# Performance work log

Hardware: AMD Instinct MI355X
Metric: run time of the kernel (lower is better)

Reference implementation:

```python
import jax, jax.numpy as jnp
import numpy as np

E = 1024
H = 16
D = E // H
B = 4
NQ = 4096
NK = 4096
LN_EPS = 1e-5


def setup_inputs() -> dict:
    key = jax.random.key(0)
    ks = jax.random.split(key, 16)
    s = 1.0 / np.sqrt(E)
    return {
        "query_embed": jax.random.normal(ks[0], (B, NQ, E), jnp.float32),
        "key_embed": jax.random.normal(ks[1], (B, NK, E), jnp.float32),
        "value": jax.random.normal(ks[2], (B, NK, E), jnp.float32),
        "Wq": jax.random.normal(ks[3], (E, E), jnp.float32) * s,
        "bq": jax.random.normal(ks[4], (E,), jnp.float32) * s,
        "Wk": jax.random.normal(ks[5], (E, E), jnp.float32) * s,
        "bk": jax.random.normal(ks[6], (E,), jnp.float32) * s,
        "Wv": jax.random.normal(ks[7], (E, E), jnp.float32) * s,
        "bv": jax.random.normal(ks[8], (E,), jnp.float32) * s,
        "Wo": jax.random.normal(ks[9], (E, E), jnp.float32) * s,
        "bo": jax.random.normal(ks[10], (E,), jnp.float32) * s,
        "gq": jnp.ones((E,), jnp.float32),
        "betaq": jnp.zeros((E,), jnp.float32),
        "gk": jnp.ones((E,), jnp.float32),
        "betak": jnp.zeros((E,), jnp.float32),
    }


def _layernorm(x, g, b):
    mu = jnp.mean(x, axis=-1, keepdims=True)
    var = jnp.mean(jnp.square(x - mu), axis=-1, keepdims=True)
    return (x - mu) * jax.lax.rsqrt(var + LN_EPS) * g + b


def reference(query_embed, key_embed, value, Wq, bq, Wk, bk, Wv, bv, Wo, bo,
              gq, betaq, gk, betak):
    Bq, Nq, _ = query_embed.shape
    _, Nk, _ = key_embed.shape
    # projections (torch Linear: x @ W.T + b) + LayerNorm
    q = _layernorm(query_embed @ Wq.T + bq, gq, betaq).reshape(Bq, Nq, H, D)
    k = _layernorm(key_embed @ Wk.T + bk, gk, betak).reshape(Bq, Nk, H, D)
    v = (value @ Wv.T + bv).reshape(Bq, Nk, H, D)
    # elu + 1 feature map
    q = jax.nn.elu(q) + 1.0  # [B, Nq, H, D]
    k = jax.nn.elu(k) + 1.0  # [B, Nk, H, D]
    # linear attention: O(N*d^2)
    kv_sum = jnp.einsum('bnhd,bnhe->bhde', k, v)        # [B, H, D, D]
    k_sum = jnp.sum(k, axis=1)                          # [B, H, D]
    num = jnp.einsum('bqhd,bhde->bqhe', q, kv_sum)      # [B, Nq, H, D]
    den = jnp.einsum('bqhd,bhd->bqh', q, k_sum)[..., None] + 1e-8
    out = (num / den).reshape(Bq, Nq, H * D)
    return out @ Wo.T + bo
```

## Files before the change

kernel.cpp:

```cpp
#include <hip/hip_runtime.h>
#include <hip/hip_bf16.h>

#define EDIM 1024
#define HHEADS 16
#define DHEAD 64
#define BB 4
#define NSEQ 4096
#define NTOK 16384
#define KVSPLIT 16

typedef unsigned short u16;
using frag8 = __attribute__((ext_vector_type(8))) short;
using facc4 = __attribute__((ext_vector_type(4))) float;

__device__ __forceinline__ float b2f(u16 u) {
  union { unsigned int i; float f; } c; c.i = ((unsigned int)u) << 16; return c.f;
}
__device__ __forceinline__ u16 f2b(float f) {
  __hip_bfloat16 h = __float2bfloat16(f);
  union { __hip_bfloat16 h; u16 u; } c; c.h = h; return c.u;
}
__device__ __forceinline__ void gl2lds16(const void* g, void* l) {
  __builtin_amdgcn_global_load_lds(
      (const __attribute__((address_space(1))) unsigned int*)g,
      (__attribute__((address_space(3))) unsigned int*)l, 16, 0, 0);
}

__global__ void detect_dtype(const u16* __restrict__ src, unsigned* __restrict__ flag) {
  const int lane = threadIdx.x;
  const unsigned u = src[(size_t)lane * 200000];
  const unsigned e = (u >> 7) & 0xFF;
  const bool inl = (u == 0) || (e >= 100 && e <= 135);
  const unsigned long long m = __ballot(inl);
  if (lane == 0) flag[0] = (__popcll(m) >= 32) ? 1u : 0u;
}

__global__ __launch_bounds__(256) void cvt_bf16(
    const void* __restrict__ src, u16* __restrict__ dst, int n,
    const unsigned* __restrict__ flag) {
  if (flag[0] == 1) return;
  const int i0 = (blockIdx.x * 256 + threadIdx.x) * 8;
  if (i0 >= n) return;
  const float4 a = ((const float4*)src)[i0 >> 2];
  const float4 b = ((const float4*)src)[(i0 >> 2) + 1];
  ushort4 lo, hi;
  lo.x = f2b(a.x); lo.y = f2b(a.y); lo.z = f2b(a.z); lo.w = f2b(a.w);
  hi.x = f2b(b.x); hi.y = f2b(b.y); hi.z = f2b(b.z); hi.w = f2b(b.w);
  ((ushort4*)dst)[i0 >> 2] = lo;
  ((ushort4*)dst)[(i0 >> 2) + 1] = hi;
}

struct Ptr8 { const void* s[8]; u16* d[8]; };
__global__ __launch_bounds__(256) void cvt8(Ptr8 p, const unsigned* __restrict__ flag) {
  const int t = blockIdx.x * 256 + threadIdx.x;
  const int v = t >> 7;
  const int i0 = (t & 127) * 8;
  const void* s = p.s[v];
  u16* d = p.d[v];
  ushort4 lo, hi;
  if (flag[0] == 0) {
    const float4 a = ((const float4*)s)[i0 >> 2];
    const float4 b = ((const float4*)s)[(i0 >> 2) + 1];
    lo.x = f2b(a.x); lo.y = f2b(a.y); lo.z = f2b(a.z); lo.w = f2b(a.w);
    hi.x = f2b(b.x); hi.y = f2b(b.y); hi.z = f2b(b.z); hi.w = f2b(b.w);
  } else {
    lo = ((const ushort4*)s)[i0 >> 2];
    hi = ((const ushort4*)s)[(i0 >> 2) + 1];
  }
  ((ushort4*)d)[i0 >> 2] = lo;
  ((ushort4*)d)[(i0 >> 2) + 1] = hi;
}

__global__ __launch_bounds__(256, 2) void gemm_bias(
    const void* __restrict__ Araw, const u16* __restrict__ Acvt,
    const void* __restrict__ Wraw, const u16* __restrict__ Wcvt,
    const u16* __restrict__ bias, u16* __restrict__ C,
    const unsigned* __restrict__ flag, int outMode)
{
  __shared__ __align__(16) u16 As[128 * 32];
  __shared__ __align__(16) u16 Bs[128 * 32];
  const int tid  = threadIdx.x;
  const int lane = tid & 63;
  const int w    = tid >> 6;
  const int wm   = w >> 1, wn = w & 1;
  const int rowBase = blockIdx.x * 128;
  const int colBase = blockIdx.y * 128;

  const bool bfw = (flag[0] == 1);
  const u16* A = bfw ? (const u16*)Araw : Acvt;
  const u16* W = bfw ? (const u16*)Wraw : Wcvt;

  facc4 acc[4][4];
#pragma unroll
  for (int i = 0; i < 4; ++i)
#pragma unroll
    for (int j = 0; j < 4; ++j) acc[i][j] = (facc4){0.f, 0.f, 0.f, 0.f};

  const int sRow = w * 32 + (lane >> 2);
  const int sCol = (lane & 3) * 8;
  const u16* Ag = A + (size_t)(rowBase + sRow) * EDIM + sCol;
  const u16* Wg = W + (size_t)(colBase + sRow) * EDIM + sCol;
  u16* AsB = As + w * 1024;
  u16* BsB = Bs + w * 1024;

  const int fr = lane & 15;
  const int kq = (lane >> 4) * 8;

  for (int k0 = 0; k0 < EDIM; k0 += 32) {
    gl2lds16(Ag + k0,            AsB);
    gl2lds16(Ag + k0 + 16*EDIM,  AsB + 512);
    gl2lds16(Wg + k0,            BsB);
    gl2lds16(Wg + k0 + 16*EDIM,  BsB + 512);
    __syncthreads();
    frag8 af[4], bf[4];
#pragma unroll
    for (int i = 0; i < 4; ++i)
      af[i] = *(const frag8*)(As + (wm * 64 + i * 16 + fr) * 32 + kq);
#pragma unroll
    for (int j = 0; j < 4; ++j)
      bf[j] = *(const frag8*)(Bs + (wn * 64 + j * 16 + fr) * 32 + kq);
#pragma unroll
    for (int i = 0; i < 4; ++i)
#pragma unroll
      for (int j = 0; j < 4; ++j)
        acc[i][j] = __builtin_amdgcn_mfma_f32_16x16x32_bf16(af[i], bf[j], acc[i][j], 0, 0, 0);
    __syncthreads();
  }

  const bool f32out = (outMode == 1) && !bfw;
  float* Cf = (float*)C;
  float bvv[4];
#pragma unroll
  for (int j = 0; j < 4; ++j)
    bvv[j] = b2f(bias[colBase + wn * 64 + j * 16 + fr]);
#pragma unroll
  for (int i = 0; i < 4; ++i) {
#pragma unroll
    for (int r = 0; r < 4; ++r) {
      const int row = rowBase + wm * 64 + i * 16 + (lane >> 4) * 4 + r;
      const size_t ro = (size_t)row * EDIM + colBase + wn * 64 + fr;
#pragma unroll
      for (int j = 0; j < 4; ++j) {
        const float val = acc[i][j][r] + bvv[j];
        if (f32out) Cf[ro + j * 16] = val;
        else        C[ro + j * 16]  = f2b(val);
      }
    }
  }
}

__global__ __launch_bounds__(256) void ln_elu(
    const u16* __restrict__ X, const u16* __restrict__ g,
    const u16* __restrict__ beta, u16* __restrict__ Y)
{
  __shared__ float wsum[4], wsq[4];
  const int row = blockIdx.x, tid = threadIdx.x;
  const ushort4 xu = ((const ushort4*)(X + (size_t)row * EDIM))[tid];
  float x[4] = { b2f(xu.x), b2f(xu.y), b2f(xu.z), b2f(xu.w) };
  float s  = x[0] + x[1] + x[2] + x[3];
  float ss = x[0]*x[0] + x[1]*x[1] + x[2]*x[2] + x[3]*x[3];
#pragma unroll
  for (int off = 32; off > 0; off >>= 1) {
    s  += __shfl_down(s,  off, 64);
    ss += __shfl_down(ss, off, 64);
  }
  if ((tid & 63) == 0) { wsum[tid >> 6] = s; wsq[tid >> 6] = ss; }
  __syncthreads();
  const float S  = wsum[0] + wsum[1] + wsum[2] + wsum[3];
  const float SS = wsq[0] + wsq[1] + wsq[2] + wsq[3];
  const float mu  = S * (1.0f / EDIM);
  const float var = SS * (1.0f / EDIM) - mu * mu;
  const float rs  = rsqrtf(var + 1e-5f);
  const ushort4 gu = ((const ushort4*)g)[tid];
  const ushort4 bu = ((const ushort4*)beta)[tid];
  float gg[4] = { b2f(gu.x), b2f(gu.y), b2f(gu.z), b2f(gu.w) };
  float bb[4] = { b2f(bu.x), b2f(bu.y), b2f(bu.z), b2f(bu.w) };
  ushort4 out;
  u16 o[4];
#pragma unroll
  for (int c = 0; c < 4; ++c) {
    float y = (x[c] - mu) * rs * gg[c] + bb[c];
    y = (y > 0.f) ? (y + 1.f) : __expf(y);
    o[c] = f2b(y);
  }
  out.x = o[0]; out.y = o[1]; out.z = o[2]; out.w = o[3];
  ((ushort4*)(Y + (size_t)row * EDIM))[tid] = out;
}

__global__ __launch_bounds__(256) void kv_partial(
    const u16* __restrict__ Km, const u16* __restrict__ V,
    float* __restrict__ partials, float* __restrict__ kspart)
{
  __shared__ __align__(16) u16 smem[2 * 64 * 130];
  u16 (*kT)[130] = (u16(*)[130])smem;
  u16 (*vT)[130] = (u16(*)[130])(smem + 64 * 130);
  float* red = (float*)smem;
  float* ksr = ((float*)smem) + 4352;

  const int split = blockIdx.x, h = blockIdx.y, b = blockIdx.z;
  const int bh = b * HHEADS + h;
  const int tid = threadIdx.x, lane = tid & 63, w = tid >> 6;
  const size_t base = (size_t)b * NSEQ * EDIM + h * DHEAD;
  const int nbase = split * (NSEQ / KVSPLIT);

  float ksacc[8] = {0, 0, 0, 0, 0, 0, 0, 0};
  facc4 acc[4][4];
#pragma unroll
  for (int i = 0; i < 4; ++i)
#pragma unroll
    for (int j = 0; j < 4; ++j) acc[i][j] = (facc4){0.f, 0.f, 0.f, 0.f};

  const int e0 = (tid & 7) * 8;
  const int nl0 = tid >> 3;
  const int fr = lane & 15;
  const int quad = lane >> 4;

  for (int c = 0; c < 2; ++c) {
    const int nchunk = nbase + c * 128;
#pragma unroll
    for (int rep = 0; rep < 4; ++rep) {
      const int n = rep * 32 + nl0;
      const uint4 kd = *(const uint4*)(Km + base + (size_t)(nchunk + n) * EDIM + e0);
      const uint4 vd = *(const uint4*)(V  + base + (size_t)(nchunk + n) * EDIM + e0);
      const u16* pk = (const u16*)&kd;
      const u16* pv = (const u16*)&vd;
#pragma unroll
      for (int ii = 0; ii < 8; ++ii) {
        kT[e0 + ii][n] = pk[ii];
        ksacc[ii] += b2f(pk[ii]);
        vT[e0 + ii][n] = pv[ii];
      }
    }
    __syncthreads();
    const int kq2 = w * 32 + quad * 8;
    frag8 af[4], bf[4];
#pragma unroll
    for (int i = 0; i < 4; ++i) af[i] = *(const frag8*)&kT[i * 16 + fr][kq2];
#pragma unroll
    for (int j = 0; j < 4; ++j) bf[j] = *(const frag8*)&vT[j * 16 + fr][kq2];
#pragma unroll
    for (int i = 0; i < 4; ++i)
#pragma unroll
      for (int j = 0; j < 4; ++j)
        acc[i][j] = __builtin_amdgcn_mfma_f32_16x16x32_bf16(af[i], bf[j], acc[i][j], 0, 0, 0);
    __syncthreads();
  }

  for (int p = 0; p < 4; ++p) {
    const int j = (w + p) & 3;
#pragma unroll
    for (int i = 0; i < 4; ++i)
#pragma unroll
      for (int r = 0; r < 4; ++r) {
        const int d = i * 16 + quad * 4 + r;
        const int e = j * 16 + fr;
        if (p == 0) red[d * 68 + e] = acc[i][j][r];
        else        red[d * 68 + e] += acc[i][j][r];
      }
    __syncthreads();
  }

  const size_t pbase = ((size_t)bh * KVSPLIT + split) * 4096;
#pragma unroll
  for (int ii = 0; ii < 16; ++ii) {
    const int idx = tid + ii * 256;
    partials[pbase + idx] = red[(idx >> 6) * 68 + (idx & 63)];
  }

#pragma unroll
  for (int ii = 0; ii < 8; ++ii) {
    ksacc[ii] += __shfl_down(ksacc[ii], 32, 64);
    ksacc[ii] += __shfl_down(ksacc[ii], 16, 64);
    ksacc[ii] += __shfl_down(ksacc[ii], 8, 64);
  }
  if (lane < 8) {
#pragma unroll
    for (int ii = 0; ii < 8; ++ii) ksr[w * 64 + lane * 8 + ii] = ksacc[ii];
  }
  __syncthreads();
  if (tid < 64)
    kspart[((size_t)bh * KVSPLIT + split) * 64 + tid] =
        ksr[tid] + ksr[64 + tid] + ksr[128 + tid] + ksr[192 + tid];
}

__global__ __launch_bounds__(256) void kv_reduce(
    const float* __restrict__ partials, const float* __restrict__ kspart,
    float* __restrict__ KV, float* __restrict__ Ks)
{
  const int qt = blockIdx.x;
  const int bh = blockIdx.y;
  const int tid = threadIdx.x;
#pragma unroll
  for (int ii = 0; ii < 4; ++ii) {
    const int idx = qt * 1024 + ii * 256 + tid;
    float s = 0.f;
#pragma unroll
    for (int sp = 0; sp < KVSPLIT; ++sp)
      s += partials[((size_t)bh * KVSPLIT + sp) * 4096 + idx];
    KV[(size_t)bh * 4096 + idx] = s;
  }
  if (qt == 0 && tid < 64) {
    float s = 0.f;
#pragma unroll
    for (int sp = 0; sp < KVSPLIT; ++sp)
      s += kspart[((size_t)bh * KVSPLIT + sp) * 64 + tid];
    Ks[bh * 64 + tid] = s;
  }
}

__global__ __launch_bounds__(256) void attn_nd(
    const u16* __restrict__ Q, const float* __restrict__ KV,
    const float* __restrict__ Ks, u16* __restrict__ O)
{
  __shared__ __align__(16) u16 kvT[64][72];
  __shared__ float ks_s[64];
  __shared__ float den_s[4][16];
  const int qt = blockIdx.x, h = blockIdx.y, b = blockIdx.z;
  const int bh = b * HHEADS + h;
  const int tid = threadIdx.x, lane = tid & 63, w = tid >> 6;
  const float* kvp = KV + (size_t)bh * 4096;
#pragma unroll
  for (int ii = 0; ii < 16; ++ii) {
    const int idx = tid + ii * 256;
    kvT[idx & 63][idx >> 6] = f2b(kvp[idx]);
  }
  if (tid < 64) ks_s[tid] = Ks[bh * 64 + tid];
  __syncthreads();

  const int fr = lane & 15;
  const int q8 = (lane >> 4) * 8;
  const u16* qp = Q + (size_t)(b * NSEQ + qt * 64 + w * 16 + fr) * EDIM + h * DHEAD;
  const frag8 a0 = *(const frag8*)(qp + q8);
  const frag8 a1 = *(const frag8*)(qp + 32 + q8);

  const u16* a0u = (const u16*)&a0;
  const u16* a1u = (const u16*)&a1;
  float den = 0.f;
#pragma unroll
  for (int j = 0; j < 8; ++j)
    den += b2f(a0u[j]) * ks_s[q8 + j] + b2f(a1u[j]) * ks_s[32 + q8 + j];
  den += __shfl_xor(den, 16, 64);
  den += __shfl_xor(den, 32, 64);
  if (lane < 16) den_s[w][lane] = den + 1e-8f;

  facc4 acc[4];
#pragma unroll
  for (int j = 0; j < 4; ++j) acc[j] = (facc4){0.f, 0.f, 0.f, 0.f};
#pragma unroll
  for (int j = 0; j < 4; ++j) {
    const frag8 b0 = *(const frag8*)&kvT[j * 16 + fr][q8];
    const frag8 b1 = *(const frag8*)&kvT[j * 16 + fr][32 + q8];
    acc[j] = __builtin_amdgcn_mfma_f32_16x16x32_bf16(a0, b0, acc[j], 0, 0, 0);
    acc[j] = __builtin_amdgcn_mfma_f32_16x16x32_bf16(a1, b1, acc[j], 0, 0, 0);
  }
  __syncthreads();
#pragma unroll
  for (int r = 0; r < 4; ++r) {
    const int rq = (lane >> 4) * 4 + r;
    const float dv = den_s[w][rq];
    const size_t orow = (size_t)(b * NSEQ + qt * 64 + w * 16 + rq) * EDIM + h * DHEAD;
#pragma unroll
    for (int j = 0; j < 4; ++j)
      O[orow + j * 16 + fr] = f2b(acc[j][r] / dv);
  }
}

extern "C" void kernel_launch(void* const* d_in, const int* in_sizes, int n_in,
                              void* d_out, int out_size, void* d_ws, size_t ws_size,
                              hipStream_t stream) {
  char* ws = (char*)d_ws;
  const size_t EH = (size_t)NTOK * EDIM;
  unsigned* flag = (unsigned*)ws;
  u16* Wqb  = (u16*)(ws + 1024);
  u16* Wkb  = Wqb + EDIM * EDIM;
  u16* Wvb  = Wkb + EDIM * EDIM;
  u16* Wob  = Wvb + EDIM * EDIM;
  u16* bqb  = Wob + EDIM * EDIM;
  u16* bkb  = bqb + 1024;
  u16* bvb  = bkb + 1024;
  u16* bob  = bvb + 1024;
  u16* gqb  = bob + 1024;
  u16* bEqb = gqb + 1024;
  u16* gkb  = bEqb + 1024;
  u16* bEkb = gkb + 1024;
  u16* Xin  = bEkb + 1024;
  u16* preQ = Xin + EH;
  u16* preK = preQ + EH;
  u16* vbuf = preK + EH;
  float* partials = (float*)(vbuf + EH);
  float* kspart   = partials + (size_t)64 * KVSPLIT * 4096;
  float* kvbuf    = kspart + (size_t)64 * KVSPLIT * 64;
  float* ksbuf    = kvbuf + (size_t)64 * 4096;

  const dim3 gg(NTOK / 128, EDIM / 128), tb(256);
  const int NW = EDIM * EDIM;

  detect_dtype<<<1, 64, 0, stream>>>((const u16*)d_in[0], flag);
  cvt_bf16<<<NW / 2048, 256, 0, stream>>>(d_in[3], Wqb, NW, flag);
  cvt_bf16<<<NW / 2048, 256, 0, stream>>>(d_in[5], Wkb, NW, flag);
  cvt_bf16<<<NW / 2048, 256, 0, stream>>>(d_in[7], Wvb, NW, flag);
  cvt_bf16<<<NW / 2048, 256, 0, stream>>>(d_in[9], Wob, NW, flag);
  Ptr8 p8;
  p8.s[0] = d_in[4];  p8.s[1] = d_in[6];  p8.s[2] = d_in[8];  p8.s[3] = d_in[10];
  p8.s[4] = d_in[11]; p8.s[5] = d_in[12]; p8.s[6] = d_in[13]; p8.s[7] = d_in[14];
  p8.d[0] = bqb; p8.d[1] = bkb; p8.d[2] = bvb; p8.d[3] = bob;
  p8.d[4] = gqb; p8.d[5] = bEqb; p8.d[6] = gkb; p8.d[7] = bEkb;
  cvt8<<<4, 256, 0, stream>>>(p8, flag);

  cvt_bf16<<<EH / 2048, 256, 0, stream>>>(d_in[0], Xin, (int)EH, flag);
  gemm_bias<<<gg, tb, 0, stream>>>(d_in[0], Xin, d_in[3], Wqb, bqb, preQ, flag, 0);
  cvt_bf16<<<EH / 2048, 256, 0, stream>>>(d_in[1], Xin, (int)EH, flag);
  gemm_bias<<<gg, tb, 0, stream>>>(d_in[1], Xin, d_in[5], Wkb, bkb, preK, flag, 0);
  cvt_bf16<<<EH / 2048, 256, 0, stream>>>(d_in[2], Xin, (int)EH, flag);
  gemm_bias<<<gg, tb, 0, stream>>>(d_in[2], Xin, d_in[7], Wvb, bvb, vbuf, flag, 0);

  ln_elu<<<NTOK, 256, 0, stream>>>(preQ, gqb, bEqb, preQ);
  ln_elu<<<NTOK, 256, 0, stream>>>(preK, gkb, bEkb, preK);

  kv_partial<<<dim3(KVSPLIT, HHEADS, BB), tb, 0, stream>>>(preK, vbuf, partials, kspart);
  kv_reduce<<<dim3(4, 64), tb, 0, stream>>>(partials, kspart, kvbuf, ksbuf);
  attn_nd<<<dim3(NSEQ / 64, HHEADS, BB), tb, 0, stream>>>(preQ, kvbuf, ksbuf, Xin);
  gemm_bias<<<gg, tb, 0, stream>>>(Xin, Xin, d_in[9], Wob, bob, (u16*)d_out, flag, 1);
}
```

Baseline: 554.2 us.

## Replace 128x128 GEMM with 256x256 tiled, double-buffered, swizzled 512-thread GEMM

Swaps the projection and output GEMM kernel for a 256x256 tile version with 8 waves, 64-wide K steps and double-buffered LDS quadrants. Global-to-LDS loads are issued across phases with explicit vmcnt waits, and XOR swizzling reduces LDS bank conflicts. A block index remap groups tiles for L2 locality. The aim is higher MFMA utilisation and more operand reuse across the four large GEMMs, at the cost of more LDS and registers per block and fragile hand scheduling.

```diff
diff --git a/kernel.cpp b/kernel.cpp
--- a/kernel.cpp
+++ b/kernel.cpp
@@ -71,61 +71,120 @@
   ((ushort4*)d)[(i0 >> 2) + 1] = hi;
 }
 
-__global__ __launch_bounds__(256, 2) void gemm_bias(
+#define STA(BUF, QM, T)                                                       \
+  gl2lds16(Ag + (size_t)(QM) * 64 * EDIM + (size_t)(T) * 64,                  \
+           AsW + (BUF) * 16384 + (QM) * 8192);                                \
+  gl2lds16(Ag + (size_t)(QM) * 64 * EDIM + 128 * EDIM + (size_t)(T) * 64,     \
+           AsW + (BUF) * 16384 + (QM) * 8192 + 4096);
+
+#define STB(BUF, QN, T)                                                       \
+  gl2lds16(Bg + (size_t)(QN) * 32 * EDIM + (size_t)(T) * 64,                  \
+           BsW + (BUF) * 16384 + (QN) * 8192);                                \
+  gl2lds16(Bg + (size_t)(QN) * 32 * EDIM + 128 * EDIM + (size_t)(T) * 64,     \
+           BsW + (BUF) * 16384 + (QN) * 8192 + 4096);
+
+#define VM(N) asm volatile("s_waitcnt vmcnt(" #N ")" ::: "memory");
+
+#define PH(BUF, QM, QN, ISSUE, TAIL)                                          \
+  {                                                                           \
+    frag8 af[4][2], bq[2][2];                                                 \
+    _Pragma("unroll") for (int i = 0; i < 4; ++i) {                           \
+      const u16* rp = &As[BUF][QM][wm * 64 + i * 16 + fr][0];                 \
+      af[i][0] = *(const frag8*)(rp + c0);                                    \
+      af[i][1] = *(const frag8*)(rp + c1);                                    \
+    }                                                                         \
+    _Pragma("unroll") for (int j = 0; j < 2; ++j) {                           \
+      const u16* rp = &Bs[BUF][QN][wn * 32 + j * 16 + fr][0];                 \
+      bq[j][0] = *(const frag8*)(rp + c0);                                    \
+      bq[j][1] = *(const frag8*)(rp + c1);                                    \
+    }                                                                         \
+    ISSUE                                                                     \
+    __builtin_amdgcn_s_barrier();                                             \
+    asm volatile("s_waitcnt lgkmcnt(0)" ::: "memory");                        \
+    __builtin_amdgcn_sched_barrier(0);                                        \
+    __builtin_amdgcn_s_setprio(1);                                            \
+    _Pragma("unroll") for (int kk = 0; kk < 2; ++kk)                          \
+      _Pragma("unroll") for (int i = 0; i < 4; ++i)                           \
+        _Pragma("unroll") for (int j = 0; j < 2; ++j)                         \
+          acc[(QM) * 4 + i][(QN) * 2 + j] =                                   \
+              __builtin_amdgcn_mfma_f32_16x16x32_bf16(                        \
+                  af[i][kk], bq[j][kk], acc[(QM) * 4 + i][(QN) * 2 + j],      \
+                  0, 0, 0);                                                   \
+    __builtin_amdgcn_s_setprio(0);                                            \
+    TAIL                                                                      \
+    __builtin_amdgcn_s_barrier();                                             \
+    __builtin_amdgcn_sched_barrier(0);                                        \
+  }
+
+__global__ __launch_bounds__(512, 2) void gemm256(
     const void* __restrict__ Araw, const u16* __restrict__ Acvt,
     const void* __restrict__ Wraw, const u16* __restrict__ Wcvt,
     const u16* __restrict__ bias, u16* __restrict__ C,
     const unsigned* __restrict__ flag, int outMode)
 {
-  __shared__ __align__(16) u16 As[128 * 32];
-  __shared__ __align__(16) u16 Bs[128 * 32];
+  __shared__ __align__(16) u16 As[2][2][128][64];
+  __shared__ __align__(16) u16 Bs[2][2][128][64];
+
   const int tid  = threadIdx.x;
   const int lane = tid & 63;
   const int w    = tid >> 6;
-  const int wm   = w >> 1, wn = w & 1;
-  const int rowBase = blockIdx.x * 128;
-  const int colBase = blockIdx.y * 128;
+  const int wm   = w >> 2;
+  const int wn   = w & 3;
+
+  const int bid0 = blockIdx.x;
+  const int bid  = (bid0 & 7) * 32 + (bid0 >> 3);
+  const int rowBase = (bid >> 2) * 256;
+  const int colBase = (bid & 3) * 256;
 
   const bool bfw = (flag[0] == 1);
-  const u16* A = bfw ? (const u16*)Araw : Acvt;
-  const u16* W = bfw ? (const u16*)Wraw : Wcvt;
-
-  facc4 acc[4][4];
-#pragma unroll
-  for (int i = 0; i < 4; ++i)
+  const u16* A  = bfw ? (const u16*)Araw : Acvt;
+  const u16* Wt = bfw ? (const u16*)Wraw : Wcvt;
+
+  const int lr = w * 8 + (lane >> 3);
+  const int sc = 8 * ((lane & 7) ^ (lane >> 3));
+  const u16* Ag = A  + (size_t)(rowBase + lr) * EDIM + sc;
+  const u16* Bg = Wt + (size_t)(colBase + (lr >> 5) * 64 + (lr & 31)) * EDIM + sc;
+  u16* AsW = &As[0][0][w * 8][0];
+  u16* BsW = &Bs[0][0][w * 8][0];
+
+  const int fr = lane & 15;
+  const int qd = lane >> 4;
+  const int sw = fr & 7;
+  const int c0 = 8 * (qd ^ sw);
+  const int c1 = 8 * ((qd + 4) ^ sw);
+
+  facc4 acc[8][4];
+#pragma unroll
+  for (int i = 0; i < 8; ++i)
 #pragma unroll
     for (int j = 0; j < 4; ++j) acc[i][j] = (facc4){0.f, 0.f, 0.f, 0.f};
 
-  const int sRow = w * 32 + (lane >> 2);
-  const int sCol = (lane & 3) * 8;
-  const u16* Ag = A + (size_t)(rowBase + sRow) * EDIM + sCol;
-  const u16* Wg = W + (size_t)(colBase + sRow) * EDIM + sCol;
-  u16* AsB = As + w * 1024;
-  u16* BsB = Bs + w * 1024;
-
-  const int fr = lane & 15;
-  const int kq = (lane >> 4) * 8;
-
-  for (int k0 = 0; k0 < EDIM; k0 += 32) {
-    gl2lds16(Ag + k0,            AsB);
-    gl2lds16(Ag + k0 + 16*EDIM,  AsB + 512);
-    gl2lds16(Wg + k0,            BsB);
-    gl2lds16(Wg + k0 + 16*EDIM,  BsB + 512);
-    __syncthreads();
-    frag8 af[4], bf[4];
-#pragma unroll
-    for (int i = 0; i < 4; ++i)
-      af[i] = *(const frag8*)(As + (wm * 64 + i * 16 + fr) * 32 + kq);
-#pragma unroll
-    for (int j = 0; j < 4; ++j)
-      bf[j] = *(const frag8*)(Bs + (wn * 64 + j * 16 + fr) * 32 + kq);
-#pragma unroll
-    for (int i = 0; i < 4; ++i)
-#pragma unroll
-      for (int j = 0; j < 4; ++j)
-        acc[i][j] = __builtin_amdgcn_mfma_f32_16x16x32_bf16(af[i], bf[j], acc[i][j], 0, 0, 0);
-    __syncthreads();
-  }
+  STA(0, 0, 0) STB(0, 0, 0) STA(0, 1, 0) STB(0, 1, 0)
+  STA(1, 0, 1) STB(1, 0, 1)
+  VM(4)
+  __builtin_amdgcn_s_barrier();
+  __builtin_amdgcn_sched_barrier(0);
+
+#pragma unroll 1
+  for (int it = 0; it < 7; ++it) {
+    const int t1 = 2 * it + 1, t2 = t1 + 1, t3 = t1 + 2;
+    PH(0, 0, 0, STA(1, 1, t1) STB(1, 1, t1), )
+    PH(0, 0, 1, , )
+    PH(0, 1, 0, STA(0, 0, t2), )
+    PH(0, 1, 1, STB(0, 0, t2), VM(4))
+    PH(1, 0, 0, STA(0, 1, t2) STB(0, 1, t2), )
+    PH(1, 0, 1, , )
+    PH(1, 1, 0, STA(1, 0, t3), )
+    PH(1, 1, 1, STB(1, 0, t3), VM(4))
+  }
+  PH(0, 0, 0, STA(1, 1, 15) STB(1, 1, 15), )
+  PH(0, 0, 1, , )
+  PH(0, 1, 0, , )
+  PH(0, 1, 1, , VM(0))
+  PH(1, 0, 0, , )
+  PH(1, 0, 1, , )
+  PH(1, 1, 0, , )
+  PH(1, 1, 1, , )
 
   const bool f32out = (outMode == 1) && !bfw;
   float* Cf = (float*)C;
@@ -134,10 +193,10 @@
   for (int j = 0; j < 4; ++j)
     bvv[j] = b2f(bias[colBase + wn * 64 + j * 16 + fr]);
 #pragma unroll
-  for (int i = 0; i < 4; ++i) {
+  for (int i = 0; i < 8; ++i) {
 #pragma unroll
     for (int r = 0; r < 4; ++r) {
-      const int row = rowBase + wm * 64 + i * 16 + (lane >> 4) * 4 + r;
+      const int row = rowBase + wm * 128 + i * 16 + qd * 4 + r;
       const size_t ro = (size_t)row * EDIM + colBase + wn * 64 + fr;
 #pragma unroll
       for (int j = 0; j < 4; ++j) {
@@ -392,7 +451,7 @@
   float* kvbuf    = kspart + (size_t)64 * KVSPLIT * 64;
   float* ksbuf    = kvbuf + (size_t)64 * 4096;
 
-  const dim3 gg(NTOK / 128, EDIM / 128), tb(256);
+  const dim3 gg(256), tb(512);
   const int NW = EDIM * EDIM;
 
   detect_dtype<<<1, 64, 0, stream>>>((const u16*)d_in[0], flag);
@@ -408,17 +467,17 @@
   cvt8<<<4, 256, 0, stream>>>(p8, flag);
 
   cvt_bf16<<<EH / 2048, 256, 0, stream>>>(d_in[0], Xin, (int)EH, flag);
-  gemm_bias<<<gg, tb, 0, stream>>>(d_in[0], Xin, d_in[3], Wqb, bqb, preQ, flag, 0);
+  gemm256<<<gg, tb, 0, stream>>>(d_in[0], Xin, d_in[3], Wqb, bqb, preQ, flag, 0);
   cvt_bf16<<<EH / 2048, 256, 0, stream>>>(d_in[1], Xin, (int)EH, flag);
-  gemm_bias<<<gg, tb, 0, stream>>>(d_in[1], Xin, d_in[5], Wkb, bkb, preK, flag, 0);
+  gemm256<<<gg, tb, 0, stream>>>(d_in[1], Xin, d_in[5], Wkb, bkb, preK, flag, 0);
   cvt_bf16<<<EH / 2048, 256, 0, stream>>>(d_in[2], Xin, (int)EH, flag);
-  gemm_bias<<<gg, tb, 0, stream>>>(d_in[2], Xin, d_in[7], Wvb, bvb, vbuf, flag, 0);
+  gemm256<<<gg, tb, 0, stream>>>(d_in[2], Xin, d_in[7], Wvb, bvb, vbuf, flag, 0);
 
   ln_elu<<<NTOK, 256, 0, stream>>>(preQ, gqb, bEqb, preQ);
   ln_elu<<<NTOK, 256, 0, stream>>>(preK, gkb, bEkb, preK);
 
-  kv_partial<<<dim3(KVSPLIT, HHEADS, BB), tb, 0, stream>>>(preK, vbuf, partials, kspart);
-  kv_reduce<<<dim3(4, 64), tb, 0, stream>>>(partials, kspart, kvbuf, ksbuf);
-  attn_nd<<<dim3(NSEQ / 64, HHEADS, BB), tb, 0, stream>>>(preQ, kvbuf, ksbuf, Xin);
-  gemm_bias<<<gg, tb, 0, stream>>>(Xin, Xin, d_in[9], Wob, bob, (u16*)d_out, flag, 1);
-}
+  kv_partial<<<dim3(KVSPLIT, HHEADS, BB), dim3(256), 0, stream>>>(preK, vbuf, partials, kspart);
+  kv_reduce<<<dim3(4, 64), dim3(256), 0, stream>>>(partials, kspart, kvbuf, ksbuf);
+  attn_nd<<<dim3(NSEQ / 64, HHEADS, BB), dim3(256), 0, stream>>>(preQ, kvbuf, ksbuf, Xin);
+  gemm256<<<gg, tb, 0, stream>>>(Xin, Xin, d_in[9], Wob, bob, (u16*)d_out, flag, 1);
+}
```

After: 540.2 us. -2.5%, faster.
